# Performance work log

Hardware: AMD Instinct MI355X
Metric: run time of the kernel (lower is better)

The kernel has to match this reference:

```python
import jax, jax.numpy as jnp
import numpy as np

N = 50000      # nodes
E = 1_600_000  # edges (avg degree 32)
H = 32         # hidden_dim
ED = 16        # edge_dim
L = 4          # num EGNN layers
F_IN = 23      # prot_in_dim
LN_EPS = 1e-5


def setup_inputs() -> dict:
    key = jax.random.key(0)
    ks = jax.random.split(key, 24)
    s = 0.1  # param init scale
    inp = {
        "node_pos": jax.random.normal(ks[0], (N, 3), jnp.float32) * 10.0,
        "node_feat": jax.random.normal(ks[1], (N, F_IN), jnp.float32),
        "edge_attr": jax.random.normal(ks[2], (E, ED), jnp.float32),
        "proj_w": jax.random.normal(ks[3], (F_IN, H), jnp.float32) * s,
        "proj_b": jnp.zeros((H,), jnp.float32),
        # phi_e: Linear(2H+ED+1 -> H), SiLU, Linear(H -> H)   [stacked over L layers]
        "pe_w1": jax.random.normal(ks[4], (L, 2 * H + ED + 1, H), jnp.float32) * s,
        "pe_b1": jnp.zeros((L, H), jnp.float32),
        "pe_w2": jax.random.normal(ks[5], (L, H, H), jnp.float32) * s,
        "pe_b2": jnp.zeros((L, H), jnp.float32),
        # phi_h: Linear(2H -> H), SiLU, Linear(H -> H)
        "ph_w1": jax.random.normal(ks[6], (L, 2 * H, H), jnp.float32) * s,
        "ph_b1": jnp.zeros((L, H), jnp.float32),
        "ph_w2": jax.random.normal(ks[7], (L, H, H), jnp.float32) * s,
        "ph_b2": jnp.zeros((L, H), jnp.float32),
        # phi_x: Linear(H -> H), SiLU, Linear(H -> 1)
        "px_w1": jax.random.normal(ks[8], (L, H, H), jnp.float32) * s,
        "px_b1": jnp.zeros((L, H), jnp.float32),
        "px_w2": jax.random.normal(ks[9], (L, H, 1), jnp.float32) * s,
        "px_b2": jnp.zeros((L, 1), jnp.float32),
        # LayerNorm per layer
        "ln_g": jnp.ones((L, H), jnp.float32),
        "ln_b": jnp.zeros((L, H), jnp.float32),
        "edge_index": jax.random.randint(ks[10], (2, E), 0, N, dtype=jnp.int32),
    }
    return inp


def _mlp2(x, w1, b1, w2, b2):
    # Linear -> SiLU -> Linear (dropout=0 / eval mode)
    return jax.nn.silu(x @ w1 + b1) @ w2 + b2


def _layernorm(x, g, b):
    mu = jnp.mean(x, axis=-1, keepdims=True)
    var = jnp.mean(jnp.square(x - mu), axis=-1, keepdims=True)
    return (x - mu) * jax.lax.rsqrt(var + LN_EPS) * g + b


def reference(node_pos, node_feat, edge_attr, proj_w, proj_b,
              pe_w1, pe_b1, pe_w2, pe_b2,
              ph_w1, ph_b1, ph_w2, ph_b2,
              px_w1, px_b1, px_w2, px_b2,
              ln_g, ln_b, edge_index):
    src = edge_index[0]
    dst = edge_index[1]
    n = node_feat.shape[0]

    h = node_feat @ proj_w + proj_b  # (N,H)
    x = node_pos                     # (N,3)

    for l in range(L):
        h_i = h[src]                 # (E,H)
        h_j = h[dst]                 # (E,H)
        x_i = x[src]                 # (E,3)
        x_j = x[dst]                 # (E,3)
        diff = x_j - x_i             # (E,3)
        dist = jnp.sqrt(jnp.sum(diff * diff, axis=-1, keepdims=True) + 1e-09)  # (E,1)

        m_in = jnp.concatenate([h_i, h_j, edge_attr, dist], axis=-1)  # (E, 2H+ED+1)
        m_ij = _mlp2(m_in, pe_w1[l], pe_b1[l], pe_w2[l], pe_b2[l])    # (E,H)

        agg = jax.ops.segment_sum(m_ij, dst, num_segments=n)          # (N,H)
        dh = _mlp2(jnp.concatenate([h, agg], axis=-1),
                   ph_w1[l], ph_b1[l], ph_w2[l], ph_b2[l])            # (N,H)
        h = _layernorm(h + dh, ln_g[l], ln_b[l])

        # coordinate update: x_j += sum_i unit(x_j - x_i) * phi_x(m_ij)
        dir_norm = jnp.linalg.norm(diff, axis=-1, keepdims=True) + 1e-09
        gate = _mlp2(m_ij, px_w1[l], px_b1[l], px_w2[l], px_b2[l])    # (E,1)
        coord_msg = (diff / dir_norm) * gate                          # (E,3)
        dx = jax.ops.segment_sum(coord_msg, dst, num_segments=n)      # (N,3)
        x = x + dx

    return h, x
```

## Files before the change

### kernel.cpp

```cpp
#include <hip/hip_runtime.h>
#include <math.h>

#define NN 50000
#define NE 1600000
#define H  32
#define ED 16
#define FIN 23
#define NL 4
#define CPAD 16

union F4 { float4 v; float f[4]; };

__device__ __forceinline__ float silu_f(float v) {
    float e = __expf(-v);
    return v * __builtin_amdgcn_rcpf(1.0f + e);
}

__device__ __forceinline__ void acc4(float hid[H], float4 hv4, const float* __restrict__ w) {
    F4 u; u.v = hv4;
    #pragma unroll
    for (int jj = 0; jj < 4; ++jj) {
        float v = u.f[jj];
        #pragma unroll
        for (int k = 0; k < H; ++k) hid[k] = fmaf(v, w[jj * H + k], hid[k]);
    }
}


__global__ __launch_bounds__(256) void k_prep(
    const float* __restrict__ pe_w2, const float* __restrict__ pe_b2,
    const float* __restrict__ px_w1, const float* __restrict__ px_b1,
    float* __restrict__ w2x, float* __restrict__ cvec)
{
    int l = blockIdx.x;
    const float* w2  = pe_w2 + (size_t)l * H * H;
    const float* xw1 = px_w1 + (size_t)l * H * H;
    int tid = threadIdx.x;
    #pragma unroll
    for (int q = 0; q < 4; ++q) {
        int idx = q * 256 + tid;
        int j = idx >> 5, k = idx & 31;
        float acc = 0.0f;
        #pragma unroll
        for (int t = 0; t < H; ++t) acc = fmaf(w2[j * H + t], xw1[t * H + k], acc);
        w2x[(size_t)l * H * H + idx] = acc;
    }
    if (tid < H) {
        const float* b2 = pe_b2 + l * H;
        float acc = px_b1[l * H + tid];
        #pragma unroll
        for (int t = 0; t < H; ++t) acc = fmaf(b2[t], xw1[t * H + tid], acc);
        cvec[l * H + tid] = acc;
    }
}


__global__ __launch_bounds__(256) void k_hist(
    const int* __restrict__ edst, int* __restrict__ cnt, int* __restrict__ rank)
{
    int e = blockIdx.x * 256 + threadIdx.x;
    if (e >= NE) return;
    rank[e] = atomicAdd(&cnt[(size_t)edst[e] * CPAD], 1);
}

__global__ __launch_bounds__(1024) void k_scan(
    const int* __restrict__ cnt, int* __restrict__ rs)
{
    __shared__ int wsum[16];
    __shared__ int s_carry;
    int t = threadIdx.x;
    int lane = t & 63, wid = t >> 6;
    if (t == 0) s_carry = 0;
    __syncthreads();
    for (int base = 0; base < NN; base += 1024) {
        int i = base + t;
        int v = (i < NN) ? cnt[(size_t)i * CPAD] : 0;
        int incl = v;
        #pragma unroll
        for (int off = 1; off < 64; off <<= 1) {
            int u = __shfl_up(incl, off, 64);
            if (lane >= off) incl += u;
        }
        if (lane == 63) wsum[wid] = incl;
        __syncthreads();
        int wpre = 0;
        #pragma unroll
        for (int w = 0; w < 16; ++w) { int ws = wsum[w]; wpre += (w < wid) ? ws : 0; }
        int carry = s_carry;
        if (i < NN) rs[i] = carry + wpre + incl - v;
        __syncthreads();
        if (t == 1023) s_carry = carry + wpre + incl;
        __syncthreads();
    }
    if (t == 0) rs[NN] = s_carry;
}

__global__ __launch_bounds__(256) void k_scatter(
    const int* __restrict__ edst, const int* __restrict__ rank,
    const int* __restrict__ rs, int* __restrict__ eid)
{
    int e = blockIdx.x * 256 + threadIdx.x;
    if (e >= NE) return;
    eid[rs[edst[e]] + rank[e]] = e;
}

__global__ __launch_bounds__(256) void k_permute(
    const int* __restrict__ eid, const float* __restrict__ ea,
    const int* __restrict__ esrc, const int* __restrict__ edst,
    float* __restrict__ ea_s, int2* __restrict__ sd_s)
{
    int slot = blockIdx.x * 256 + threadIdx.x;
    if (slot >= NE) return;
    int e = eid[slot];
    const float4* src4 = (const float4*)(ea + (size_t)e * ED);
    float4* dst4 = (float4*)(ea_s + (size_t)slot * ED);
    #pragma unroll
    for (int j = 0; j < ED / 4; ++j) dst4[j] = src4[j];
    int2 sd; sd.x = esrc[e]; sd.y = edst[e];
    sd_s[slot] = sd;
}


__global__ __launch_bounds__(256) void proj2(
    const float* __restrict__ feat, const float* __restrict__ W,
    const float* __restrict__ bias, const float* __restrict__ pew1,
    float* __restrict__ h, float* __restrict__ a, float* __restrict__ b)
{
    int n = blockIdx.x * 256 + threadIdx.x;
    if (n >= NN) return;
    float acc[H];
    #pragma unroll
    for (int k = 0; k < H; ++k) acc[k] = bias[k];
    #pragma unroll 1
    for (int j = 0; j < FIN; ++j) {
        float v = feat[n * FIN + j];
        const float* w = W + j * H;
        #pragma unroll
        for (int k = 0; k < H; ++k) acc[k] = fmaf(v, w[k], acc[k]);
    }
    float4* h4 = (float4*)(h + (size_t)n * H);
    #pragma unroll
    for (int k4 = 0; k4 < H / 4; ++k4) {
        float4 o;
        o.x = acc[4*k4+0]; o.y = acc[4*k4+1]; o.z = acc[4*k4+2]; o.w = acc[4*k4+3];
        h4[k4] = o;
    }
    float pa[H];
    #pragma unroll
    for (int k = 0; k < H; ++k) pa[k] = 0.0f;
    #pragma unroll 1
    for (int j = 0; j < H; ++j) {
        float v = acc[j];
        const float* w = pew1 + j * H;
        #pragma unroll
        for (int k = 0; k < H; ++k) pa[k] = fmaf(v, w[k], pa[k]);
    }
    float4* a4 = (float4*)(a + (size_t)n * H);
    #pragma unroll
    for (int k4 = 0; k4 < H / 4; ++k4) {
        float4 o;
        o.x = pa[4*k4+0]; o.y = pa[4*k4+1]; o.z = pa[4*k4+2]; o.w = pa[4*k4+3];
        a4[k4] = o;
    }
    #pragma unroll
    for (int k = 0; k < H; ++k) pa[k] = 0.0f;
    #pragma unroll 1
    for (int j = 0; j < H; ++j) {
        float v = acc[j];
        const float* w = pew1 + (H + j) * H;
        #pragma unroll
        for (int k = 0; k < H; ++k) pa[k] = fmaf(v, w[k], pa[k]);
    }
    float4* b4 = (float4*)(b + (size_t)n * H);
    #pragma unroll
    for (int k4 = 0; k4 < H / 4; ++k4) {
        float4 o;
        o.x = pa[4*k4+0]; o.y = pa[4*k4+1]; o.z = pa[4*k4+2]; o.w = pa[4*k4+3];
        b4[k4] = o;
    }
}


#define LSTRIDE 37

__global__ __launch_bounds__(256) void egnn_edge4(
    const float* __restrict__ a, const float* __restrict__ b,
    const float* __restrict__ x,
    const float* __restrict__ ea_s, const int2* __restrict__ sd_s,
    const float* __restrict__ w1, const float* __restrict__ b1,
    const float* __restrict__ w2x, const float* __restrict__ cvec,
    const float* __restrict__ xw2, const float* __restrict__ xb2,
    float* __restrict__ agg, float* __restrict__ dxb)
{
    __shared__ float lds[256 * LSTRIDE];
    __shared__ int s_start[4][66];
    __shared__ int s_dstv[4][64];
    __shared__ int s_nseg[4];

    int tid = threadIdx.x;
    int w = tid >> 6, lane = tid & 63;
    int slot = blockIdx.x * 256 + tid;

    int2 sd = sd_s[slot];
    int s = sd.x, d = sd.y;

    float hid[H];
    const float4* av = (const float4*)(a + (size_t)s * H);
    const float4* bv = (const float4*)(b + (size_t)d * H);
    #pragma unroll
    for (int k4 = 0; k4 < H / 4; ++k4) {
        F4 ua, ub; ua.v = av[k4]; ub.v = bv[k4];
        #pragma unroll
        for (int jj = 0; jj < 4; ++jj)
            hid[4*k4+jj] = b1[4*k4+jj] + ua.f[jj] + ub.f[jj];
    }

    const float4* eav = (const float4*)(ea_s + (size_t)slot * ED);
    #pragma unroll 1
    for (int j4 = 0; j4 < ED / 4; ++j4)
        acc4(hid, eav[j4], w1 + (2 * H + j4 * 4) * H);

    float xi0 = x[3*s+0], xi1 = x[3*s+1], xi2 = x[3*s+2];
    float xj0 = x[3*d+0], xj1 = x[3*d+1], xj2 = x[3*d+2];
    float d0 = xj0 - xi0, d1 = xj1 - xi1, d2 = xj2 - xi2;
    float sq = d0*d0 + d1*d1 + d2*d2;
    float dist = __builtin_amdgcn_sqrtf(sq + 1e-9f);
    {
        const float* wl = w1 + (2 * H + ED) * H;
        #pragma unroll
        for (int k = 0; k < H; ++k) hid[k] = fmaf(dist, wl[k], hid[k]);
    }

    float sarr[H];
    float gh[H];
    #pragma unroll
    for (int k = 0; k < H; ++k) gh[k] = cvec[k];
    #pragma unroll
    for (int j = 0; j < H; ++j) {
        float v = silu_f(hid[j]);
        sarr[j] = v;
        const float* ww = w2x + j * H;
        #pragma unroll
        for (int k = 0; k < H; ++k) gh[k] = fmaf(v, ww[k], gh[k]);
    }

    float gate = xb2[0];
    #pragma unroll
    for (int j = 0; j < H; ++j) gate = fmaf(silu_f(gh[j]), xw2[j], gate);
    float scale = gate * __builtin_amdgcn_rcpf(__builtin_amdgcn_sqrtf(sq) + 1e-9f);

    float* row = &lds[tid * LSTRIDE];
    #pragma unroll
    for (int k = 0; k < H; ++k) row[k] = sarr[k];
    row[32] = d0 * scale; row[33] = d1 * scale; row[34] = d2 * scale;

    int dprev = __shfl_up(d, 1, 64);
    bool flag = (lane == 0) || (d != dprev);
    unsigned long long ball = __ballot(flag);
    unsigned long long mask_le = (lane == 63) ? ~0ull : ((1ull << (lane + 1)) - 1ull);
    int segid = __popcll(ball & mask_le) - 1;
    if (flag) { s_start[w][segid] = lane; s_dstv[w][segid] = d; }
    if (lane == 0) {
        int ns = __popcll(ball);
        s_start[w][ns] = 64;
        s_nseg[w] = ns;
    }
    __syncthreads();

    int nseg = s_nseg[w];
    const float* wrows = &lds[(w * 64) * LSTRIDE];
    int sub = lane >> 5, col = lane & 31;
    #pragma unroll 1
    for (int sg = sub; sg < nseg; sg += 2) {
        int r0 = s_start[w][sg], r1 = s_start[w][sg + 1];
        float v = 0.0f;
        #pragma unroll 1
        for (int r = r0; r < r1; ++r) v += wrows[r * LSTRIDE + col];
        unsafeAtomicAdd(&agg[(size_t)s_dstv[w][sg] * H + col], v);
    }
    #pragma unroll 1
    for (int j = lane; j < nseg * 4; j += 64) {
        int sg = j >> 2, c = j & 3;
        if (c < 3) {
            int r0 = s_start[w][sg], r1 = s_start[w][sg + 1];
            float v = 0.0f;
            #pragma unroll 1
            for (int r = r0; r < r1; ++r) v += wrows[r * LSTRIDE + 32 + c];
            unsafeAtomicAdd(&dxb[(size_t)s_dstv[w][sg] * 4 + c], v);
        }
    }
}


__global__ __launch_bounds__(256) void egnn_node4(
    const float* __restrict__ h, const float* __restrict__ agg,
    const float* __restrict__ xin, const float* __restrict__ dxb,
    const int* __restrict__ rs,
    const float* __restrict__ ew2, const float* __restrict__ eb2,
    const float* __restrict__ w1, const float* __restrict__ b1,
    const float* __restrict__ w2, const float* __restrict__ b2,
    const float* __restrict__ lng, const float* __restrict__ lnb,
    const float* __restrict__ nxtw1, int last,
    float* __restrict__ hout, float* __restrict__ xout,
    float* __restrict__ aout, float* __restrict__ bout)
{
    int n = blockIdx.x * 256 + threadIdx.x;
    if (n >= NN) return;
    const float4* h4 = (const float4*)(h + (size_t)n * H);
    const float4* a4 = (const float4*)(agg + (size_t)n * H);

    float degf = (float)(rs[n + 1] - rs[n]);
    float ma[H];
    #pragma unroll
    for (int k = 0; k < H; ++k) ma[k] = degf * eb2[k];
    #pragma unroll 1
    for (int j4 = 0; j4 < H / 4; ++j4)
        acc4(ma, a4[j4], ew2 + (j4 * 4) * H);

    float hv[H];
    float hid[H];
    #pragma unroll
    for (int k = 0; k < H; ++k) hid[k] = b1[k];
    #pragma unroll 1
    for (int j4 = 0; j4 < H / 4; ++j4) {
        F4 u; u.v = h4[j4];
        #pragma unroll
        for (int jj = 0; jj < 4; ++jj) hv[4*j4+jj] = u.f[jj];
        acc4(hid, u.v, w1 + (j4 * 4) * H);
    }
    #pragma unroll
    for (int j = 0; j < H; ++j) {
        float v = ma[j];
        const float* ww = w1 + (H + j) * H;
        #pragma unroll
        for (int k = 0; k < H; ++k) hid[k] = fmaf(v, ww[k], hid[k]);
    }

    float dh[H];
    #pragma unroll
    for (int k = 0; k < H; ++k) dh[k] = b2[k];
    #pragma unroll
    for (int j = 0; j < H; ++j) {
        float v = silu_f(hid[j]);
        const float* ww = w2 + j * H;
        #pragma unroll
        for (int k = 0; k < H; ++k) dh[k] = fmaf(v, ww[k], dh[k]);
    }

    float y[H];
    float mu = 0.0f;
    #pragma unroll
    for (int k = 0; k < H; ++k) { y[k] = hv[k] + dh[k]; mu += y[k]; }
    mu *= (1.0f / H);
    float var = 0.0f;
    #pragma unroll
    for (int k = 0; k < H; ++k) { float t = y[k] - mu; var += t * t; }
    var *= (1.0f / H);
    float rstd = rsqrtf(var + 1e-5f);

    float hn[H];
    #pragma unroll
    for (int k = 0; k < H; ++k) hn[k] = (y[k] - mu) * rstd * lng[k] + lnb[k];

    float4* ho4 = (float4*)(hout + (size_t)n * H);
    #pragma unroll
    for (int k4 = 0; k4 < H / 4; ++k4) {
        float4 o;
        o.x = hn[4*k4+0]; o.y = hn[4*k4+1]; o.z = hn[4*k4+2]; o.w = hn[4*k4+3];
        ho4[k4] = o;
    }

    xout[3*n+0] = xin[3*n+0] + dxb[(size_t)n * 4 + 0];
    xout[3*n+1] = xin[3*n+1] + dxb[(size_t)n * 4 + 1];
    xout[3*n+2] = xin[3*n+2] + dxb[(size_t)n * 4 + 2];

    if (!last) {
        float pa[H];
        #pragma unroll
        for (int k = 0; k < H; ++k) pa[k] = 0.0f;
        #pragma unroll 1
        for (int j = 0; j < H; ++j) {
            float v = hn[j];
            const float* ww = nxtw1 + j * H;
            #pragma unroll
            for (int k = 0; k < H; ++k) pa[k] = fmaf(v, ww[k], pa[k]);
        }
        float4* ao4 = (float4*)(aout + (size_t)n * H);
        #pragma unroll
        for (int k4 = 0; k4 < H / 4; ++k4) {
            float4 o;
            o.x = pa[4*k4+0]; o.y = pa[4*k4+1]; o.z = pa[4*k4+2]; o.w = pa[4*k4+3];
            ao4[k4] = o;
        }
        #pragma unroll
        for (int k = 0; k < H; ++k) pa[k] = 0.0f;
        #pragma unroll 1
        for (int j = 0; j < H; ++j) {
            float v = hn[j];
            const float* ww = nxtw1 + (H + j) * H;
            #pragma unroll
            for (int k = 0; k < H; ++k) pa[k] = fmaf(v, ww[k], pa[k]);
        }
        float4* bo4 = (float4*)(bout + (size_t)n * H);
        #pragma unroll
        for (int k4 = 0; k4 < H / 4; ++k4) {
            float4 o;
            o.x = pa[4*k4+0]; o.y = pa[4*k4+1]; o.z = pa[4*k4+2]; o.w = pa[4*k4+3];
            bo4[k4] = o;
        }
    }
}

extern "C" void kernel_launch(void* const* d_in, const int* in_sizes, int n_in,
                              void* d_out, int out_size, void* d_ws, size_t ws_size,
                              hipStream_t stream) {
    const float* node_pos  = (const float*)d_in[0];
    const float* node_feat = (const float*)d_in[1];
    const float* edge_attr = (const float*)d_in[2];
    const float* proj_w    = (const float*)d_in[3];
    const float* proj_b    = (const float*)d_in[4];
    const float* pe_w1     = (const float*)d_in[5];
    const float* pe_b1     = (const float*)d_in[6];
    const float* pe_w2     = (const float*)d_in[7];
    const float* pe_b2     = (const float*)d_in[8];
    const float* ph_w1     = (const float*)d_in[9];
    const float* ph_b1     = (const float*)d_in[10];
    const float* ph_w2     = (const float*)d_in[11];
    const float* ph_b2     = (const float*)d_in[12];
    const float* px_w1     = (const float*)d_in[13];
    const float* px_b1     = (const float*)d_in[14];
    const float* px_w2     = (const float*)d_in[15];
    const float* px_b2     = (const float*)d_in[16];
    const float* ln_g      = (const float*)d_in[17];
    const float* ln_b      = (const float*)d_in[18];
    const int*   eidx      = (const int*)d_in[19];
    const int*   esrc      = eidx;
    const int*   edst      = eidx + NE;

    float* out_h = (float*)d_out;
    float* out_x = out_h + (size_t)NN * H;

    size_t off = 0;
    float* ea_s = (float*)d_ws;                off += (size_t)NE * ED;
    int2*  sd_s = (int2*)((float*)d_ws + off); off += (size_t)NE * 2;
    float* abuf = (float*)d_ws + off;          off += (size_t)NN * H;
    float* bbuf = (float*)d_ws + off;          off += (size_t)NN * H;
    float* h_a  = (float*)d_ws + off;          off += (size_t)NN * H;
    float* h_b  = (float*)d_ws + off;          off += (size_t)NN * H;
    float* x_a  = (float*)d_ws + off;          off += (size_t)NN * 3;
    float* x_b  = (float*)d_ws + off;          off += (size_t)NN * 3;
    float* agg  = (float*)d_ws + off;          off += (size_t)NN * H;
    float* dxb  = (float*)d_ws + off;          off += (size_t)NN * 4;
    float* w2x  = (float*)d_ws + off;          off += (size_t)NL * H * H;
    float* cvec = (float*)d_ws + off;          off += (size_t)NL * H;
    int*   cnt  = (int*)((float*)d_ws + off);  off += (size_t)NN * CPAD;
    int*   rs   = (int*)((float*)d_ws + off);  off += NN + 4;
    int*   rank = (int*)((float*)d_ws + off);  off += NE;
    int*   eid  = (int*)((float*)d_ws + off);  off += NE;

    dim3 nblk((NN + 255) / 256), eblk(NE / 256);

    hipMemsetAsync(cnt, 0, (size_t)NN * CPAD * sizeof(int), stream);
    k_hist<<<eblk, 256, 0, stream>>>(edst, cnt, rank);
    k_scan<<<1, 1024, 0, stream>>>(cnt, rs);
    k_scatter<<<eblk, 256, 0, stream>>>(edst, rank, rs, eid);
    k_permute<<<eblk, 256, 0, stream>>>(eid, edge_attr, esrc, edst, ea_s, sd_s);
    k_prep<<<dim3(NL), 256, 0, stream>>>(pe_w2, pe_b2, px_w1, px_b1, w2x, cvec);

    proj2<<<nblk, 256, 0, stream>>>(node_feat, proj_w, proj_b, pe_w1, h_a, abuf, bbuf);

    const float* hcur = h_a;
    const float* xcur = node_pos;
    float* hbufs[2] = { h_b, h_a };
    float* xbufs[2] = { x_a, x_b };

    for (int l = 0; l < NL; ++l) {
        hipMemsetAsync(agg, 0, (size_t)NN * (H + 4) * sizeof(float), stream);
        egnn_edge4<<<eblk, 256, 0, stream>>>(abuf, bbuf, xcur, ea_s, sd_s,
            pe_w1 + (size_t)l * (2*H + ED + 1) * H, pe_b1 + l * H,
            w2x + (size_t)l * H * H,               cvec + l * H,
            px_w2 + (size_t)l * H,                 px_b2 + l,
            agg, dxb);
        float* ho = (l == NL - 1) ? out_h : hbufs[l & 1];
        float* xo = (l == NL - 1) ? out_x : xbufs[l & 1];
        int last = (l == NL - 1);
        const float* nxtw1 = last ? pe_w1 : (pe_w1 + (size_t)(l + 1) * (2*H + ED + 1) * H);
        egnn_node4<<<nblk, 256, 0, stream>>>(hcur, agg, xcur, dxb, rs,
            pe_w2 + (size_t)l * H * H, pe_b2 + l * H,
            ph_w1 + (size_t)l * 2 * H * H, ph_b1 + l * H,
            ph_w2 + (size_t)l * H * H,     ph_b2 + l * H,
            ln_g + l * H, ln_b + l * H,
            nxtw1, last, ho, xo, abuf, bbuf);
        hcur = ho;
        xcur = xo;
    }
}
```

Before: 1.158 ms.

## Pack edge indices, pad positions to float4, fp16 LDS staging, fuse scatter+permute

Merges the edge scatter and permute kernels into one pass that writes sorted edge attributes and a packed 16-bit src/dst word. Node positions are stored as float4 so each edge loads one vector per endpoint. The per-edge silu activations are staged in shared memory as half2, roughly halving LDS usage to raise occupancy, at the cost of reduced precision in the message aggregation. Packing indices into 16 bits relies on the node count fitting in 16 bits.

```diff
diff --git a/kernel.cpp b/kernel.cpp
--- a/kernel.cpp
+++ b/kernel.cpp
@@ -1,4 +1,5 @@
 #include <hip/hip_runtime.h>
+#include <hip/hip_fp16.h>
 #include <math.h>
 
 #define NN 50000
@@ -8,6 +9,7 @@
 #define FIN 23
 #define NL 4
 #define CPAD 16
+#define LW 19
 
 union F4 { float4 v; float f[4]; };
 
@@ -95,36 +97,30 @@
     if (t == 0) rs[NN] = s_carry;
 }
 
-__global__ __launch_bounds__(256) void k_scatter(
-    const int* __restrict__ edst, const int* __restrict__ rank,
-    const int* __restrict__ rs, int* __restrict__ eid)
+__global__ __launch_bounds__(256) void k_scatter2(
+    const int* __restrict__ esrc, const int* __restrict__ edst,
+    const int* __restrict__ rank, const int* __restrict__ rs,
+    const float* __restrict__ ea,
+    float* __restrict__ ea_s, unsigned int* __restrict__ sdp)
 {
     int e = blockIdx.x * 256 + threadIdx.x;
     if (e >= NE) return;
-    eid[rs[edst[e]] + rank[e]] = e;
-}
-
-__global__ __launch_bounds__(256) void k_permute(
-    const int* __restrict__ eid, const float* __restrict__ ea,
-    const int* __restrict__ esrc, const int* __restrict__ edst,
-    float* __restrict__ ea_s, int2* __restrict__ sd_s)
-{
-    int slot = blockIdx.x * 256 + threadIdx.x;
-    if (slot >= NE) return;
-    int e = eid[slot];
+    int s = esrc[e], d = edst[e];
+    int slot = rs[d] + rank[e];
     const float4* src4 = (const float4*)(ea + (size_t)e * ED);
     float4* dst4 = (float4*)(ea_s + (size_t)slot * ED);
     #pragma unroll
     for (int j = 0; j < ED / 4; ++j) dst4[j] = src4[j];
-    int2 sd; sd.x = esrc[e]; sd.y = edst[e];
-    sd_s[slot] = sd;
+    sdp[slot] = (unsigned int)s | ((unsigned int)d << 16);
 }
 
 
 __global__ __launch_bounds__(256) void proj2(
-    const float* __restrict__ feat, const float* __restrict__ W,
-    const float* __restrict__ bias, const float* __restrict__ pew1,
-    float* __restrict__ h, float* __restrict__ a, float* __restrict__ b)
+    const float* __restrict__ feat, const float* __restrict__ pos,
+    const float* __restrict__ W, const float* __restrict__ bias,
+    const float* __restrict__ pew1,
+    float* __restrict__ h, float* __restrict__ a, float* __restrict__ b,
+    float4* __restrict__ xp)
 {
     int n = blockIdx.x * 256 + threadIdx.x;
     if (n >= NN) return;
@@ -178,21 +174,22 @@
         o.x = pa[4*k4+0]; o.y = pa[4*k4+1]; o.z = pa[4*k4+2]; o.w = pa[4*k4+3];
         b4[k4] = o;
     }
-}
-
-
-#define LSTRIDE 37
-
-__global__ __launch_bounds__(256) void egnn_edge4(
+    float4 xo;
+    xo.x = pos[3*n+0]; xo.y = pos[3*n+1]; xo.z = pos[3*n+2]; xo.w = 0.0f;
+    xp[n] = xo;
+}
+
+
+__global__ __launch_bounds__(256) void egnn_edge5(
     const float* __restrict__ a, const float* __restrict__ b,
-    const float* __restrict__ x,
-    const float* __restrict__ ea_s, const int2* __restrict__ sd_s,
+    const float4* __restrict__ xp,
+    const float* __restrict__ ea_s, const unsigned int* __restrict__ sdp,
     const float* __restrict__ w1, const float* __restrict__ b1,
     const float* __restrict__ w2x, const float* __restrict__ cvec,
     const float* __restrict__ xw2, const float* __restrict__ xb2,
     float* __restrict__ agg, float* __restrict__ dxb)
 {
-    __shared__ float lds[256 * LSTRIDE];
+    __shared__ unsigned int ldsu[256 * LW];
     __shared__ int s_start[4][66];
     __shared__ int s_dstv[4][64];
     __shared__ int s_nseg[4];
@@ -201,8 +198,8 @@
     int w = tid >> 6, lane = tid & 63;
     int slot = blockIdx.x * 256 + tid;
 
-    int2 sd = sd_s[slot];
-    int s = sd.x, d = sd.y;
+    unsigned int sd = sdp[slot];
+    int s = (int)(sd & 0xffffu), d = (int)(sd >> 16);
 
     float hid[H];
     const float4* av = (const float4*)(a + (size_t)s * H);
@@ -220,9 +217,9 @@
     for (int j4 = 0; j4 < ED / 4; ++j4)
         acc4(hid, eav[j4], w1 + (2 * H + j4 * 4) * H);
 
-    float xi0 = x[3*s+0], xi1 = x[3*s+1], xi2 = x[3*s+2];
-    float xj0 = x[3*d+0], xj1 = x[3*d+1], xj2 = x[3*d+2];
-    float d0 = xj0 - xi0, d1 = xj1 - xi1, d2 = xj2 - xi2;
+    float4 xi = xp[s];
+    float4 xj = xp[d];
+    float d0 = xj.x - xi.x, d1 = xj.y - xi.y, d2 = xj.z - xi.z;
     float sq = d0*d0 + d1*d1 + d2*d2;
     float dist = __builtin_amdgcn_sqrtf(sq + 1e-9f);
     {
@@ -249,10 +246,15 @@
     for (int j = 0; j < H; ++j) gate = fmaf(silu_f(gh[j]), xw2[j], gate);
     float scale = gate * __builtin_amdgcn_rcpf(__builtin_amdgcn_sqrtf(sq) + 1e-9f);
 
-    float* row = &lds[tid * LSTRIDE];
-    #pragma unroll
-    for (int k = 0; k < H; ++k) row[k] = sarr[k];
-    row[32] = d0 * scale; row[33] = d1 * scale; row[34] = d2 * scale;
+    unsigned int* row = &ldsu[tid * LW];
+    #pragma unroll
+    for (int k2 = 0; k2 < 16; ++k2) {
+        __half2 hh = __floats2half2_rn(sarr[2*k2], sarr[2*k2+1]);
+        row[k2] = *reinterpret_cast<unsigned int*>(&hh);
+    }
+    row[16] = __float_as_uint(d0 * scale);
+    row[17] = __float_as_uint(d1 * scale);
+    row[18] = __float_as_uint(d2 * scale);
 
     int dprev = __shfl_up(d, 1, 64);
     bool flag = (lane == 0) || (d != dprev);
@@ -268,14 +270,18 @@
     __syncthreads();
 
     int nseg = s_nseg[w];
-    const float* wrows = &lds[(w * 64) * LSTRIDE];
+    const unsigned int* wrows = &ldsu[(w * 64) * LW];
     int sub = lane >> 5, col = lane & 31;
+    int word = col >> 1, sh = (col & 1) * 16;
     #pragma unroll 1
     for (int sg = sub; sg < nseg; sg += 2) {
         int r0 = s_start[w][sg], r1 = s_start[w][sg + 1];
         float v = 0.0f;
         #pragma unroll 1
-        for (int r = r0; r < r1; ++r) v += wrows[r * LSTRIDE + col];
+        for (int r = r0; r < r1; ++r) {
+            unsigned int u = wrows[r * LW + word];
+            v += __half2float(__ushort_as_half((unsigned short)(u >> sh)));
+        }
         unsafeAtomicAdd(&agg[(size_t)s_dstv[w][sg] * H + col], v);
     }
     #pragma unroll 1
@@ -285,16 +291,16 @@
             int r0 = s_start[w][sg], r1 = s_start[w][sg + 1];
             float v = 0.0f;
             #pragma unroll 1
-            for (int r = r0; r < r1; ++r) v += wrows[r * LSTRIDE + 32 + c];
+            for (int r = r0; r < r1; ++r) v += __uint_as_float(wrows[r * LW + 16 + c]);
             unsafeAtomicAdd(&dxb[(size_t)s_dstv[w][sg] * 4 + c], v);
         }
     }
 }
 
 
-__global__ __launch_bounds__(256) void egnn_node4(
+__global__ __launch_bounds__(256) void egnn_node5(
     const float* __restrict__ h, const float* __restrict__ agg,
-    const float* __restrict__ xin, const float* __restrict__ dxb,
+    const float4* __restrict__ xin, const float* __restrict__ dxb,
     const int* __restrict__ rs,
     const float* __restrict__ ew2, const float* __restrict__ eb2,
     const float* __restrict__ w1, const float* __restrict__ b1,
@@ -370,9 +376,16 @@
         ho4[k4] = o;
     }
 
-    xout[3*n+0] = xin[3*n+0] + dxb[(size_t)n * 4 + 0];
-    xout[3*n+1] = xin[3*n+1] + dxb[(size_t)n * 4 + 1];
-    xout[3*n+2] = xin[3*n+2] + dxb[(size_t)n * 4 + 2];
+    float4 xi = xin[n];
+    float nx0 = xi.x + dxb[(size_t)n * 4 + 0];
+    float nx1 = xi.y + dxb[(size_t)n * 4 + 1];
+    float nx2 = xi.z + dxb[(size_t)n * 4 + 2];
+    if (last) {
+        xout[3*n+0] = nx0; xout[3*n+1] = nx1; xout[3*n+2] = nx2;
+    } else {
+        float4 o; o.x = nx0; o.y = nx1; o.z = nx2; o.w = 0.0f;
+        ((float4*)xout)[n] = o;
+    }
 
     if (!last) {
         float pa[H];
@@ -442,13 +455,13 @@
 
     size_t off = 0;
     float* ea_s = (float*)d_ws;                off += (size_t)NE * ED;
-    int2*  sd_s = (int2*)((float*)d_ws + off); off += (size_t)NE * 2;
+    unsigned int* sdp = (unsigned int*)((float*)d_ws + off); off += NE;
     float* abuf = (float*)d_ws + off;          off += (size_t)NN * H;
     float* bbuf = (float*)d_ws + off;          off += (size_t)NN * H;
     float* h_a  = (float*)d_ws + off;          off += (size_t)NN * H;
     float* h_b  = (float*)d_ws + off;          off += (size_t)NN * H;
-    float* x_a  = (float*)d_ws + off;          off += (size_t)NN * 3;
-    float* x_b  = (float*)d_ws + off;          off += (size_t)NN * 3;
+    float4* xp_a = (float4*)((float*)d_ws + off); off += (size_t)NN * 4;
+    float4* xp_b = (float4*)((float*)d_ws + off); off += (size_t)NN * 4;
     float* agg  = (float*)d_ws + off;          off += (size_t)NN * H;
     float* dxb  = (float*)d_ws + off;          off += (size_t)NN * 4;
     float* w2x  = (float*)d_ws + off;          off += (size_t)NL * H * H;
@@ -456,42 +469,41 @@
     int*   cnt  = (int*)((float*)d_ws + off);  off += (size_t)NN * CPAD;
     int*   rs   = (int*)((float*)d_ws + off);  off += NN + 4;
     int*   rank = (int*)((float*)d_ws + off);  off += NE;
-    int*   eid  = (int*)((float*)d_ws + off);  off += NE;
 
     dim3 nblk((NN + 255) / 256), eblk(NE / 256);
 
     hipMemsetAsync(cnt, 0, (size_t)NN * CPAD * sizeof(int), stream);
     k_hist<<<eblk, 256, 0, stream>>>(edst, cnt, rank);
     k_scan<<<1, 1024, 0, stream>>>(cnt, rs);
-    k_scatter<<<eblk, 256, 0, stream>>>(edst, rank, rs, eid);
-    k_permute<<<eblk, 256, 0, stream>>>(eid, edge_attr, esrc, edst, ea_s, sd_s);
+    k_scatter2<<<eblk, 256, 0, stream>>>(esrc, edst, rank, rs, edge_attr, ea_s, sdp);
     k_prep<<<dim3(NL), 256, 0, stream>>>(pe_w2, pe_b2, px_w1, px_b1, w2x, cvec);
 
-    proj2<<<nblk, 256, 0, stream>>>(node_feat, proj_w, proj_b, pe_w1, h_a, abuf, bbuf);
+    proj2<<<nblk, 256, 0, stream>>>(node_feat, node_pos, proj_w, proj_b, pe_w1,
+                                    h_a, abuf, bbuf, xp_a);
 
     const float* hcur = h_a;
-    const float* xcur = node_pos;
+    const float4* xcur = xp_a;
     float* hbufs[2] = { h_b, h_a };
-    float* xbufs[2] = { x_a, x_b };
+    float4* xbufs[2] = { xp_b, xp_a };
 
     for (int l = 0; l < NL; ++l) {
         hipMemsetAsync(agg, 0, (size_t)NN * (H + 4) * sizeof(float), stream);
-        egnn_edge4<<<eblk, 256, 0, stream>>>(abuf, bbuf, xcur, ea_s, sd_s,
+        egnn_edge5<<<eblk, 256, 0, stream>>>(abuf, bbuf, xcur, ea_s, sdp,
             pe_w1 + (size_t)l * (2*H + ED + 1) * H, pe_b1 + l * H,
             w2x + (size_t)l * H * H,               cvec + l * H,
             px_w2 + (size_t)l * H,                 px_b2 + l,
             agg, dxb);
-        float* ho = (l == NL - 1) ? out_h : hbufs[l & 1];
-        float* xo = (l == NL - 1) ? out_x : xbufs[l & 1];
         int last = (l == NL - 1);
+        float* ho = last ? out_h : hbufs[l & 1];
+        float* xo = last ? out_x : (float*)xbufs[l & 1];
         const float* nxtw1 = last ? pe_w1 : (pe_w1 + (size_t)(l + 1) * (2*H + ED + 1) * H);
-        egnn_node4<<<nblk, 256, 0, stream>>>(hcur, agg, xcur, dxb, rs,
+        egnn_node5<<<nblk, 256, 0, stream>>>(hcur, agg, xcur, dxb, rs,
             pe_w2 + (size_t)l * H * H, pe_b2 + l * H,
             ph_w1 + (size_t)l * 2 * H * H, ph_b1 + l * H,
             ph_w2 + (size_t)l * H * H,     ph_b2 + l * H,
             ln_g + l * H, ln_b + l * H,
             nxtw1, last, ho, xo, abuf, bbuf);
         hcur = ho;
-        xcur = xo;
-    }
-}
+        xcur = xbufs[l & 1];
+    }
+}
```

After: 1.160 ms. Within noise of the previous version (+0.2%).
